# Kernel tuning notes

Measured on AMD Instinct MI355X. Metric: run time of the kernel, lower is better.

## Reference

```python
import jax, jax.numpy as jnp
import numpy as np

B, S, H, NREL = 4, 512, 256, 99


def setup_inputs() -> dict:
    key = jax.random.key(0)
    ks = jax.random.split(key, 6)
    return {
        "queries": jax.random.normal(ks[0], (B, S, H), dtype=jnp.float32),
        "keys": jax.random.normal(ks[1], (B, S, H), dtype=jnp.float32),
        "relations": jax.random.randint(ks[2], (B, S, S), 0, NREL, dtype=jnp.int64),
        "Wq": jax.random.normal(ks[3], (H, H), dtype=jnp.float32) * 0.02,
        "bq": jnp.zeros((H,), dtype=jnp.float32),
        "Wk": jax.random.normal(ks[4], (H, H), dtype=jnp.float32) * 0.02,
        "bk": jnp.zeros((H,), dtype=jnp.float32),
        "rel_emb": jax.random.normal(ks[5], (NREL, H), dtype=jnp.float32) * 0.02,
    }


def reference(queries, keys, relations, Wq, bq, Wk, bk, rel_emb):
    # Linear projections (torch Linear: x @ W.T + b)
    q = queries @ Wq.T + bq        # [B, Sq, H]
    k = keys @ Wk.T + bk           # [B, Sk, H]
    r = rel_emb[relations]         # [B, Sq, Sk, H]

    # single head: qk^T + q . r^T, scaled
    qk = jnp.einsum("bqd,bkd->bqk", q, k)       # [B, Sq, Sk]
    qr = jnp.einsum("bqd,bqkd->bqk", q, r)      # [B, Sq, Sk]
    scale = 1.0 / jnp.sqrt(jnp.asarray(q.shape[-1], q.dtype))
    logits = (qk + qr) * scale
    return jax.nn.softmax(logits, axis=-1)       # squeezed head dim -> [B, Sq, Sk]
```

## Files before the change

kernel.cpp:

```cpp
#include <hip/hip_runtime.h>

typedef __attribute__((ext_vector_type(8))) short bf8;
typedef __attribute__((ext_vector_type(4))) float f4;

#define QBF  0
#define KBF  524288
#define REBF 1048576

static __device__ __forceinline__ short bfr(float x) {
    union { float f; unsigned u; } v; v.f = x;
    return (short)((v.u + 0x7FFF + ((v.u >> 16) & 1)) >> 16);
}
static __device__ __forceinline__ bf8 pack8(float4 a, float4 b) {
    bf8 r;
    r[0] = bfr(a.x); r[1] = bfr(a.y); r[2] = bfr(a.z); r[3] = bfr(a.w);
    r[4] = bfr(b.x); r[5] = bfr(b.y); r[6] = bfr(b.z); r[7] = bfr(b.w);
    return r;
}

__global__ __launch_bounds__(256) void proj_kernel(const float* __restrict__ queries,
                                                   const float* __restrict__ keys,
                                                   const float* __restrict__ bq,
                                                   const float* __restrict__ bk,
                                                   const float* __restrict__ Wq,
                                                   const float* __restrict__ Wk,
                                                   const float* __restrict__ rel_emb,
                                                   short* __restrict__ ws) {
    __shared__ short w_l[64 * 264];
    int blk = blockIdx.x;
    int tid = threadIdx.x;

    if (blk >= 256) {
        int idx = ((blk - 256) * 256 + tid) * 16;
        float4 a = make_float4(0.f, 0.f, 0.f, 0.f), b = a, c = a, d = a;
        if ((idx >> 8) < 99) {
            const float4* s = (const float4*)(rel_emb + idx);
            a = s[0]; b = s[1]; c = s[2]; d = s[3];
        }
        *(bf8*)(ws + REBF + idx) = pack8(a, b);
        *(bf8*)(ws + REBF + idx + 8) = pack8(c, d);
        return;
    }

    int mat = blk >> 7;
    int t = blk & 127;
    int m0 = (t >> 2) * 64;
    int n0 = (t & 3) * 64;
    const float* x = mat ? keys : queries;
    const float* W = mat ? Wk : Wq;
    const float* bias = mat ? bk : bq;
    short* outp = ws + (mat ? KBF : QBF);

    int w = tid >> 6;
    int lane = tid & 63;
    int n15 = lane & 15, quad = lane >> 4;

#pragma unroll
    for (int cc = 0; cc < 8; cc++) {
        int chunk = cc * 256 + tid;
        int row = chunk >> 5, col8 = chunk & 31;
        const float4* s = (const float4*)(W + (n0 + row) * 256 + col8 * 8);
        *(bf8*)&w_l[row * 264 + col8 * 8] = pack8(s[0], s[1]);
    }

    int mrow = m0 + w * 16 + n15;
    bf8 afr[8];
#pragma unroll
    for (int kk = 0; kk < 8; kk++) {
        const float4* ap = (const float4*)(x + mrow * 256 + kk * 32 + quad * 8);
        afr[kk] = pack8(ap[0], ap[1]);
    }
    __syncthreads();

    f4 z = {0.f, 0.f, 0.f, 0.f};
    f4 c[4] = {z, z, z, z};
#pragma unroll
    for (int nt = 0; nt < 4; nt++) {
        const short* wr = &w_l[(nt * 16 + n15) * 264 + quad * 8];
#pragma unroll
        for (int kk = 0; kk < 8; kk++) {
            bf8 bfrag = *(const bf8*)(wr + kk * 32);
            c[nt] = __builtin_amdgcn_mfma_f32_16x16x32_bf16(afr[kk], bfrag, c[nt], 0, 0, 0);
        }
    }

    int mbase = m0 + w * 16 + quad * 4;
#pragma unroll
    for (int nt = 0; nt < 4; nt++) {
        int col = n0 + nt * 16 + n15;
        float bv = bias[col];
#pragma unroll
        for (int reg = 0; reg < 4; reg++)
            outp[(mbase + reg) * 256 + col] = bfr(c[nt][reg] + bv);
    }
}

__global__ __launch_bounds__(512) void attn_kernel(const int* __restrict__ relations,
                                                   const short* __restrict__ ws,
                                                   float* __restrict__ out) {
    __shared__ float qr_l[16][112];
    __shared__ float red_m[16][8];
    __shared__ float red_s[16][8];

    int blk = blockIdx.x;
    int b = blk >> 6;
    int i0 = (blk & 63) * 8;
    int gi0 = b * 512 + i0;
    int w = threadIdx.x >> 6;
    int lane = threadIdx.x & 63;
    int n15 = lane & 15, quad = lane >> 4;
    int j0 = w * 64;

    const int* rb = relations + (gi0 + (quad & 1) * 4) * 512 + j0 + n15;
    int rv[4][4];
#pragma unroll
    for (int reg = 0; reg < 4; reg++)
#pragma unroll
        for (int nt = 0; nt < 4; nt++)
            rv[nt][reg] = rb[reg * 512 + nt * 16];

    const short* qbf = ws + QBF;
    const short* kbf = ws + KBF;
    const short* rebf = ws + REBF;

    int arow = gi0 + (n15 & 7);
    bf8 afr[8];
#pragma unroll
    for (int kk = 0; kk < 8; kk++)
        afr[kk] = *(const bf8*)(qbf + arow * 256 + kk * 32 + quad * 8);

    f4 z = {0.f, 0.f, 0.f, 0.f};
    f4 c[4] = {z, z, z, z};
#pragma unroll
    for (int nt = 0; nt < 4; nt++) {
        int krow = b * 512 + j0 + nt * 16 + n15;
        const short* kr = kbf + krow * 256 + quad * 8;
#pragma unroll
        for (int kk = 0; kk < 8; kk++) {
            bf8 bfrag = *(const bf8*)(kr + kk * 32);
            c[nt] = __builtin_amdgcn_mfma_f32_16x16x32_bf16(afr[kk], bfrag, c[nt], 0, 0, 0);
        }
    }

    if (w < 7) {
        f4 cq = z;
        const short* rr = rebf + (w * 16 + n15) * 256 + quad * 8;
#pragma unroll
        for (int kk = 0; kk < 8; kk++) {
            bf8 bfrag = *(const bf8*)(rr + kk * 32);
            cq = __builtin_amdgcn_mfma_f32_16x16x32_bf16(afr[kk], bfrag, cq, 0, 0, 0);
        }
#pragma unroll
        for (int reg = 0; reg < 4; reg++)
            qr_l[quad * 4 + reg][w * 16 + n15] = cq[reg];
    }
    __syncthreads();

    const float scale = 0.0625f;
    float lg[4][4];
#pragma unroll
    for (int nt = 0; nt < 4; nt++)
#pragma unroll
        for (int reg = 0; reg < 4; reg++)
            lg[nt][reg] = (c[nt][reg] + qr_l[quad * 4 + reg][rv[nt][reg]]) * scale;

    float pm[4];
#pragma unroll
    for (int reg = 0; reg < 4; reg++) {
        float m = fmaxf(fmaxf(lg[0][reg], lg[1][reg]), fmaxf(lg[2][reg], lg[3][reg]));
#pragma unroll
        for (int d = 1; d <= 8; d <<= 1) m = fmaxf(m, __shfl_xor(m, d, 64));
        pm[reg] = m;
    }
    if (n15 == 0)
#pragma unroll
        for (int reg = 0; reg < 4; reg++) red_m[quad * 4 + reg][w] = pm[reg];
    __syncthreads();
    float M[4];
#pragma unroll
    for (int reg = 0; reg < 4; reg++) {
        f4 a0 = *(const f4*)&red_m[quad * 4 + reg][0];
        f4 a1 = *(const f4*)&red_m[quad * 4 + reg][4];
        M[reg] = fmaxf(fmaxf(fmaxf(a0[0], a0[1]), fmaxf(a0[2], a0[3])),
                       fmaxf(fmaxf(a1[0], a1[1]), fmaxf(a1[2], a1[3])));
    }

    float ps[4];
#pragma unroll
    for (int reg = 0; reg < 4; reg++) {
        float s = 0.f;
#pragma unroll
        for (int nt = 0; nt < 4; nt++) {
            float e = __expf(lg[nt][reg] - M[reg]);
            lg[nt][reg] = e;
            s += e;
        }
#pragma unroll
        for (int d = 1; d <= 8; d <<= 1) s += __shfl_xor(s, d, 64);
        ps[reg] = s;
    }
    if (n15 == 0)
#pragma unroll
        for (int reg = 0; reg < 4; reg++) red_s[quad * 4 + reg][w] = ps[reg];
    __syncthreads();
    float inv[4];
#pragma unroll
    for (int reg = 0; reg < 4; reg++) {
        f4 a0 = *(const f4*)&red_s[quad * 4 + reg][0];
        f4 a1 = *(const f4*)&red_s[quad * 4 + reg][4];
        inv[reg] = 1.f / (a0[0] + a0[1] + a0[2] + a0[3] + a1[0] + a1[1] + a1[2] + a1[3]);
    }

    if (quad < 2) {
        float* ob = out + (gi0 + quad * 4) * 512 + j0 + n15;
#pragma unroll
        for (int reg = 0; reg < 4; reg++)
#pragma unroll
            for (int nt = 0; nt < 4; nt++)
                ob[reg * 512 + nt * 16] = lg[nt][reg] * inv[reg];
    }
}

extern "C" void kernel_launch(void* const* d_in, const int* in_sizes, int n_in,
                              void* d_out, int out_size, void* d_ws, size_t ws_size,
                              hipStream_t stream) {
    const float* queries = (const float*)d_in[0];
    const float* keys = (const float*)d_in[1];
    const int* relations = (const int*)d_in[2];
    const float* Wq = (const float*)d_in[3];
    const float* bq = (const float*)d_in[4];
    const float* Wk = (const float*)d_in[5];
    const float* bk = (const float*)d_in[6];
    const float* rel_emb = (const float*)d_in[7];
    short* wss = (short*)d_ws;
    float* out = (float*)d_out;

    hipLaunchKernelGGL(proj_kernel, dim3(263), dim3(256), 0, stream,
                       queries, keys, bq, bk, Wq, Wk, rel_emb, wss);
    hipLaunchKernelGGL(attn_kernel, dim3(256), dim3(512), 0, stream, relations, wss, out);
}
```

Before: 91.98 us.

## Fuse projection and attention kernels into one cooperative launch with grid sync

Merges the projection kernel and the attention/softmax kernel into a single cooperative kernel of 256 blocks x 512 threads. A grid-wide barrier separates the projection phase from the attention phase, and shared memory is reused through a union. The projection work is redistributed so each block of 8 waves covers a 64x64 output tile with 2 n-tiles per wave, and the rel_emb conversion is spread over the first blocks. This removes one kernel launch and its inter-kernel gap, at the cost of a grid sync and the cooperative-launch overhead.

After: 205.2 us. +123.1%, slower.

```diff
diff --git a/kernel.cpp b/kernel.cpp
--- a/kernel.cpp
+++ b/kernel.cpp
@@ -1,4 +1,7 @@
 #include <hip/hip_runtime.h>
+#include <hip/hip_cooperative_groups.h>
+
+namespace cg = cooperative_groups;
 
 typedef __attribute__((ext_vector_type(8))) short bf8;
 typedef __attribute__((ext_vector_type(4))) float f4;
@@ -18,206 +21,211 @@
     return r;
 }
 
-__global__ __launch_bounds__(256) void proj_kernel(const float* __restrict__ queries,
-                                                   const float* __restrict__ keys,
-                                                   const float* __restrict__ bq,
-                                                   const float* __restrict__ bk,
-                                                   const float* __restrict__ Wq,
-                                                   const float* __restrict__ Wk,
-                                                   const float* __restrict__ rel_emb,
-                                                   short* __restrict__ ws) {
-    __shared__ short w_l[64 * 264];
+__global__ __launch_bounds__(512) void fused_kernel(
+    const float* __restrict__ queries, const float* __restrict__ keys,
+    const float* __restrict__ bq, const float* __restrict__ bk,
+    const float* __restrict__ Wq, const float* __restrict__ Wk,
+    const float* __restrict__ rel_emb, const int* __restrict__ relations,
+    short* __restrict__ ws, float* __restrict__ out)
+{
+    __shared__ union SM {
+        short w_l[64 * 264];
+        struct {
+            float qr_l[16][112];
+            float red_m[16][8];
+            float red_s[16][8];
+        } a;
+    } sm;
+
     int blk = blockIdx.x;
     int tid = threadIdx.x;
-
-    if (blk >= 256) {
-        int idx = ((blk - 256) * 256 + tid) * 16;
-        float4 a = make_float4(0.f, 0.f, 0.f, 0.f), b = a, c = a, d = a;
-        if ((idx >> 8) < 99) {
-            const float4* s = (const float4*)(rel_emb + idx);
-            a = s[0]; b = s[1]; c = s[2]; d = s[3];
-        }
-        *(bf8*)(ws + REBF + idx) = pack8(a, b);
-        *(bf8*)(ws + REBF + idx + 8) = pack8(c, d);
-        return;
-    }
-
-    int mat = blk >> 7;
-    int t = blk & 127;
-    int m0 = (t >> 2) * 64;
-    int n0 = (t & 3) * 64;
-    const float* x = mat ? keys : queries;
-    const float* W = mat ? Wk : Wq;
-    const float* bias = mat ? bk : bq;
-    short* outp = ws + (mat ? KBF : QBF);
-
     int w = tid >> 6;
     int lane = tid & 63;
     int n15 = lane & 15, quad = lane >> 4;
 
-#pragma unroll
-    for (int cc = 0; cc < 8; cc++) {
-        int chunk = cc * 256 + tid;
-        int row = chunk >> 5, col8 = chunk & 31;
-        const float4* s = (const float4*)(W + (n0 + row) * 256 + col8 * 8);
-        *(bf8*)&w_l[row * 264 + col8 * 8] = pack8(s[0], s[1]);
+    {
+        int g = blk * 512 + tid;
+        if (g < 1792) {
+            int idx = g * 16;
+            float4 a = make_float4(0.f, 0.f, 0.f, 0.f), b = a, c2 = a, d = a;
+            if ((idx >> 8) < 99) {
+                const float4* s = (const float4*)(rel_emb + idx);
+                a = s[0]; b = s[1]; c2 = s[2]; d = s[3];
+            }
+            *(bf8*)(ws + REBF + idx) = pack8(a, b);
+            *(bf8*)(ws + REBF + idx + 8) = pack8(c2, d);
+        }
     }
 
-    int mrow = m0 + w * 16 + n15;
-    bf8 afr[8];
-#pragma unroll
-    for (int kk = 0; kk < 8; kk++) {
-        const float4* ap = (const float4*)(x + mrow * 256 + kk * 32 + quad * 8);
-        afr[kk] = pack8(ap[0], ap[1]);
+    {
+        int mat = blk >> 7;
+        int t = blk & 127;
+        int m0 = (t >> 2) * 64;
+        int n0 = (t & 3) * 64;
+        const float* x = mat ? keys : queries;
+        const float* W = mat ? Wk : Wq;
+        const float* bias = mat ? bk : bq;
+        short* outp = ws + (mat ? KBF : QBF);
+
+        int wr = w & 3, wc = w >> 2;
+
+#pragma unroll
+        for (int cc = 0; cc < 4; cc++) {
+            int chunk = cc * 512 + tid;
+            int row = chunk >> 5, col8 = chunk & 31;
+            const float4* s = (const float4*)(W + (n0 + row) * 256 + col8 * 8);
+            *(bf8*)&sm.w_l[row * 264 + col8 * 8] = pack8(s[0], s[1]);
+        }
+
+        int mrow = m0 + wr * 16 + n15;
+        bf8 afr[8];
+#pragma unroll
+        for (int kk = 0; kk < 8; kk++) {
+            const float4* ap = (const float4*)(x + mrow * 256 + kk * 32 + quad * 8);
+            afr[kk] = pack8(ap[0], ap[1]);
+        }
+        __syncthreads();
+
+        f4 z = {0.f, 0.f, 0.f, 0.f};
+        f4 c[2] = {z, z};
+#pragma unroll
+        for (int nt = 0; nt < 2; nt++) {
+            const short* wrp = &sm.w_l[(wc * 32 + nt * 16 + n15) * 264 + quad * 8];
+#pragma unroll
+            for (int kk = 0; kk < 8; kk++) {
+                bf8 bfrag = *(const bf8*)(wrp + kk * 32);
+                c[nt] = __builtin_amdgcn_mfma_f32_16x16x32_bf16(afr[kk], bfrag, c[nt], 0, 0, 0);
+            }
+        }
+
+        int mbase = m0 + wr * 16 + quad * 4;
+#pragma unroll
+        for (int nt = 0; nt < 2; nt++) {
+            int col = n0 + wc * 32 + nt * 16 + n15;
+            float bv = bias[col];
+#pragma unroll
+            for (int reg = 0; reg < 4; reg++)
+                outp[(mbase + reg) * 256 + col] = bfr(c[nt][reg] + bv);
+        }
     }
-    __syncthreads();
-
-    f4 z = {0.f, 0.f, 0.f, 0.f};
-    f4 c[4] = {z, z, z, z};
-#pragma unroll
-    for (int nt = 0; nt < 4; nt++) {
-        const short* wr = &w_l[(nt * 16 + n15) * 264 + quad * 8];
-#pragma unroll
-        for (int kk = 0; kk < 8; kk++) {
-            bf8 bfrag = *(const bf8*)(wr + kk * 32);
-            c[nt] = __builtin_amdgcn_mfma_f32_16x16x32_bf16(afr[kk], bfrag, c[nt], 0, 0, 0);
-        }
-    }
-
-    int mbase = m0 + w * 16 + quad * 4;
-#pragma unroll
-    for (int nt = 0; nt < 4; nt++) {
-        int col = n0 + nt * 16 + n15;
-        float bv = bias[col];
+
+    __threadfence();
+    cg::this_grid().sync();
+
+    {
+        int b = blk >> 6;
+        int i0 = (blk & 63) * 8;
+        int gi0 = b * 512 + i0;
+        int j0 = w * 64;
+
+        const int* rb = relations + (gi0 + (quad & 1) * 4) * 512 + j0 + n15;
+        int rv[4][4];
 #pragma unroll
         for (int reg = 0; reg < 4; reg++)
-            outp[(mbase + reg) * 256 + col] = bfr(c[nt][reg] + bv);
-    }
-}
-
-__global__ __launch_bounds__(512) void attn_kernel(const int* __restrict__ relations,
-                                                   const short* __restrict__ ws,
-                                                   float* __restrict__ out) {
-    __shared__ float qr_l[16][112];
-    __shared__ float red_m[16][8];
-    __shared__ float red_s[16][8];
-
-    int blk = blockIdx.x;
-    int b = blk >> 6;
-    int i0 = (blk & 63) * 8;
-    int gi0 = b * 512 + i0;
-    int w = threadIdx.x >> 6;
-    int lane = threadIdx.x & 63;
-    int n15 = lane & 15, quad = lane >> 4;
-    int j0 = w * 64;
-
-    const int* rb = relations + (gi0 + (quad & 1) * 4) * 512 + j0 + n15;
-    int rv[4][4];
-#pragma unroll
-    for (int reg = 0; reg < 4; reg++)
+#pragma unroll
+            for (int nt = 0; nt < 4; nt++)
+                rv[nt][reg] = rb[reg * 512 + nt * 16];
+
+        const short* qbf = ws + QBF;
+        const short* kbf = ws + KBF;
+        const short* rebf = ws + REBF;
+
+        int arow = gi0 + (n15 & 7);
+        bf8 afr[8];
+#pragma unroll
+        for (int kk = 0; kk < 8; kk++)
+            afr[kk] = *(const bf8*)(qbf + arow * 256 + kk * 32 + quad * 8);
+
+        f4 z = {0.f, 0.f, 0.f, 0.f};
+        f4 c[4] = {z, z, z, z};
+#pragma unroll
+        for (int nt = 0; nt < 4; nt++) {
+            int krow = b * 512 + j0 + nt * 16 + n15;
+            const short* kr = kbf + krow * 256 + quad * 8;
+#pragma unroll
+            for (int kk = 0; kk < 8; kk++) {
+                bf8 bfrag = *(const bf8*)(kr + kk * 32);
+                c[nt] = __builtin_amdgcn_mfma_f32_16x16x32_bf16(afr[kk], bfrag, c[nt], 0, 0, 0);
+            }
+        }
+
+        if (w < 7) {
+            f4 cq = z;
+            const short* rr = rebf + (w * 16 + n15) * 256 + quad * 8;
+#pragma unroll
+            for (int kk = 0; kk < 8; kk++) {
+                bf8 bfrag = *(const bf8*)(rr + kk * 32);
+                cq = __builtin_amdgcn_mfma_f32_16x16x32_bf16(afr[kk], bfrag, cq, 0, 0, 0);
+            }
+#pragma unroll
+            for (int reg = 0; reg < 4; reg++)
+                sm.a.qr_l[quad * 4 + reg][w * 16 + n15] = cq[reg];
+        }
+        __syncthreads();
+
+        const float scale = 0.0625f;
+        float lg[4][4];
 #pragma unroll
         for (int nt = 0; nt < 4; nt++)
-            rv[nt][reg] = rb[reg * 512 + nt * 16];
-
-    const short* qbf = ws + QBF;
-    const short* kbf = ws + KBF;
-    const short* rebf = ws + REBF;
-
-    int arow = gi0 + (n15 & 7);
-    bf8 afr[8];
-#pragma unroll
-    for (int kk = 0; kk < 8; kk++)
-        afr[kk] = *(const bf8*)(qbf + arow * 256 + kk * 32 + quad * 8);
-
-    f4 z = {0.f, 0.f, 0.f, 0.f};
-    f4 c[4] = {z, z, z, z};
-#pragma unroll
-    for (int nt = 0; nt < 4; nt++) {
-        int krow = b * 512 + j0 + nt * 16 + n15;
-        const short* kr = kbf + krow * 256 + quad * 8;
-#pragma unroll
-        for (int kk = 0; kk < 8; kk++) {
-            bf8 bfrag = *(const bf8*)(kr + kk * 32);
-            c[nt] = __builtin_amdgcn_mfma_f32_16x16x32_bf16(afr[kk], bfrag, c[nt], 0, 0, 0);
-        }
-    }
-
-    if (w < 7) {
-        f4 cq = z;
-        const short* rr = rebf + (w * 16 + n15) * 256 + quad * 8;
-#pragma unroll
-        for (int kk = 0; kk < 8; kk++) {
-            bf8 bfrag = *(const bf8*)(rr + kk * 32);
-            cq = __builtin_amdgcn_mfma_f32_16x16x32_bf16(afr[kk], bfrag, cq, 0, 0, 0);
-        }
-#pragma unroll
-        for (int reg = 0; reg < 4; reg++)
-            qr_l[quad * 4 + reg][w * 16 + n15] = cq[reg];
-    }
-    __syncthreads();
-
-    const float scale = 0.0625f;
-    float lg[4][4];
-#pragma unroll
-    for (int nt = 0; nt < 4; nt++)
-#pragma unroll
-        for (int reg = 0; reg < 4; reg++)
-            lg[nt][reg] = (c[nt][reg] + qr_l[quad * 4 + reg][rv[nt][reg]]) * scale;
-
-    float pm[4];
-#pragma unroll
-    for (int reg = 0; reg < 4; reg++) {
-        float m = fmaxf(fmaxf(lg[0][reg], lg[1][reg]), fmaxf(lg[2][reg], lg[3][reg]));
-#pragma unroll
-        for (int d = 1; d <= 8; d <<= 1) m = fmaxf(m, __shfl_xor(m, d, 64));
-        pm[reg] = m;
-    }
-    if (n15 == 0)
-#pragma unroll
-        for (int reg = 0; reg < 4; reg++) red_m[quad * 4 + reg][w] = pm[reg];
-    __syncthreads();
-    float M[4];
-#pragma unroll
-    for (int reg = 0; reg < 4; reg++) {
-        f4 a0 = *(const f4*)&red_m[quad * 4 + reg][0];
-        f4 a1 = *(const f4*)&red_m[quad * 4 + reg][4];
-        M[reg] = fmaxf(fmaxf(fmaxf(a0[0], a0[1]), fmaxf(a0[2], a0[3])),
-                       fmaxf(fmaxf(a1[0], a1[1]), fmaxf(a1[2], a1[3])));
-    }
-
-    float ps[4];
-#pragma unroll
-    for (int reg = 0; reg < 4; reg++) {
-        float s = 0.f;
-#pragma unroll
-        for (int nt = 0; nt < 4; nt++) {
-            float e = __expf(lg[nt][reg] - M[reg]);
-            lg[nt][reg] = e;
-            s += e;
-        }
-#pragma unroll
-        for (int d = 1; d <= 8; d <<= 1) s += __shfl_xor(s, d, 64);
-        ps[reg] = s;
-    }
-    if (n15 == 0)
-#pragma unroll
-        for (int reg = 0; reg < 4; reg++) red_s[quad * 4 + reg][w] = ps[reg];
-    __syncthreads();
-    float inv[4];
-#pragma unroll
-    for (int reg = 0; reg < 4; reg++) {
-        f4 a0 = *(const f4*)&red_s[quad * 4 + reg][0];
-        f4 a1 = *(const f4*)&red_s[quad * 4 + reg][4];
-        inv[reg] = 1.f / (a0[0] + a0[1] + a0[2] + a0[3] + a1[0] + a1[1] + a1[2] + a1[3]);
-    }
-
-    if (quad < 2) {
-        float* ob = out + (gi0 + quad * 4) * 512 + j0 + n15;
-#pragma unroll
-        for (int reg = 0; reg < 4; reg++)
-#pragma unroll
-            for (int nt = 0; nt < 4; nt++)
-                ob[reg * 512 + nt * 16] = lg[nt][reg] * inv[reg];
+#pragma unroll
+            for (int reg = 0; reg < 4; reg++)
+                lg[nt][reg] = (c[nt][reg] + sm.a.qr_l[quad * 4 + reg][rv[nt][reg]]) * scale;
+
+        float pm[4];
+#pragma unroll
+        for (int reg = 0; reg < 4; reg++) {
+            float m = fmaxf(fmaxf(lg[0][reg], lg[1][reg]), fmaxf(lg[2][reg], lg[3][reg]));
+#pragma unroll
+            for (int d = 1; d <= 8; d <<= 1) m = fmaxf(m, __shfl_xor(m, d, 64));
+            pm[reg] = m;
+        }
+        if (n15 == 0)
+#pragma unroll
+            for (int reg = 0; reg < 4; reg++) sm.a.red_m[quad * 4 + reg][w] = pm[reg];
+        __syncthreads();
+        float M[4];
+#pragma unroll
+        for (int reg = 0; reg < 4; reg++) {
+            f4 a0 = *(const f4*)&sm.a.red_m[quad * 4 + reg][0];
+            f4 a1 = *(const f4*)&sm.a.red_m[quad * 4 + reg][4];
+            M[reg] = fmaxf(fmaxf(fmaxf(a0[0], a0[1]), fmaxf(a0[2], a0[3])),
+                           fmaxf(fmaxf(a1[0], a1[1]), fmaxf(a1[2], a1[3])));
+        }
+
+        float ps[4];
+#pragma unroll
+        for (int reg = 0; reg < 4; reg++) {
+            float s = 0.f;
+#pragma unroll
+            for (int nt = 0; nt < 4; nt++) {
+                float e = __expf(lg[nt][reg] - M[reg]);
+                lg[nt][reg] = e;
+                s += e;
+            }
+#pragma unroll
+            for (int d = 1; d <= 8; d <<= 1) s += __shfl_xor(s, d, 64);
+            ps[reg] = s;
+        }
+        if (n15 == 0)
+#pragma unroll
+            for (int reg = 0; reg < 4; reg++) sm.a.red_s[quad * 4 + reg][w] = ps[reg];
+        __syncthreads();
+        float inv[4];
+#pragma unroll
+        for (int reg = 0; reg < 4; reg++) {
+            f4 a0 = *(const f4*)&sm.a.red_s[quad * 4 + reg][0];
+            f4 a1 = *(const f4*)&sm.a.red_s[quad * 4 + reg][4];
+            inv[reg] = 1.f / (a0[0] + a0[1] + a0[2] + a0[3] + a1[0] + a1[1] + a1[2] + a1[3]);
+        }
+
+        if (quad < 2) {
+            float* ob = out + (gi0 + quad * 4) * 512 + j0 + n15;
+#pragma unroll
+            for (int reg = 0; reg < 4; reg++)
+#pragma unroll
+                for (int nt = 0; nt < 4; nt++)
+                    ob[reg * 512 + nt * 16] = lg[nt][reg] * inv[reg];
+        }
     }
 }
 
@@ -235,7 +243,8 @@
     short* wss = (short*)d_ws;
     float* out = (float*)d_out;
 
-    hipLaunchKernelGGL(proj_kernel, dim3(263), dim3(256), 0, stream,
-                       queries, keys, bq, bk, Wq, Wk, rel_emb, wss);
-    hipLaunchKernelGGL(attn_kernel, dim3(256), dim3(512), 0, stream, relations, wss, out);
-}
+    void* args[] = {(void*)&queries, (void*)&keys, (void*)&bq, (void*)&bk,
+                    (void*)&Wq, (void*)&Wk, (void*)&rel_emb, (void*)&relations,
+                    (void*)&wss, (void*)&out};
+    hipLaunchCooperativeKernel((void*)fused_kernel, dim3(256), dim3(512), args, 0, stream);
+}
```

## Shrink projection and attention tiles to launch more blocks

Applied to the files above, without the earlier changes.

The projection GEMM moves from 64x64 to 32x32 output tiles, with each of four waves computing one 16x16 tile, so the grid grows from 263 to 1031 blocks. The attention kernel handles 4 query rows per block instead of 8, doubling the grid to 512 blocks. The 4 rows are replicated across the MFMA's 16 rows, and each quad writes the column tile matching its index. The aim is to fill more CUs and cut per-block latency. The cost is redundant MFMA work and about twice the total K/rel-embedding reads from L2.

After: 129.4 us. 40.7% more time.

```diff
diff --git a/kernel.cpp b/kernel.cpp
--- a/kernel.cpp
+++ b/kernel.cpp
@@ -26,12 +26,12 @@
                                                    const float* __restrict__ Wk,
                                                    const float* __restrict__ rel_emb,
                                                    short* __restrict__ ws) {
-    __shared__ short w_l[64 * 264];
+    __shared__ short w_l[32 * 264];
     int blk = blockIdx.x;
     int tid = threadIdx.x;
 
-    if (blk >= 256) {
-        int idx = ((blk - 256) * 256 + tid) * 16;
+    if (blk >= 1024) {
+        int idx = ((blk - 1024) * 256 + tid) * 16;
         float4 a = make_float4(0.f, 0.f, 0.f, 0.f), b = a, c = a, d = a;
         if ((idx >> 8) < 99) {
             const float4* s = (const float4*)(rel_emb + idx);
@@ -42,10 +42,10 @@
         return;
     }
 
-    int mat = blk >> 7;
-    int t = blk & 127;
-    int m0 = (t >> 2) * 64;
-    int n0 = (t & 3) * 64;
+    int mat = blk >> 9;
+    int t = blk & 511;
+    int m0 = (t >> 3) * 32;
+    int n0 = (t & 7) * 32;
     const float* x = mat ? keys : queries;
     const float* W = mat ? Wk : Wq;
     const float* bias = mat ? bk : bq;
@@ -54,16 +54,17 @@
     int w = tid >> 6;
     int lane = tid & 63;
     int n15 = lane & 15, quad = lane >> 4;
-
-#pragma unroll
-    for (int cc = 0; cc < 8; cc++) {
+    int wr = w & 1, wc = w >> 1;
+
+#pragma unroll
+    for (int cc = 0; cc < 4; cc++) {
         int chunk = cc * 256 + tid;
         int row = chunk >> 5, col8 = chunk & 31;
         const float4* s = (const float4*)(W + (n0 + row) * 256 + col8 * 8);
         *(bf8*)&w_l[row * 264 + col8 * 8] = pack8(s[0], s[1]);
     }
 
-    int mrow = m0 + w * 16 + n15;
+    int mrow = m0 + wr * 16 + n15;
     bf8 afr[8];
 #pragma unroll
     for (int kk = 0; kk < 8; kk++) {
@@ -72,27 +73,20 @@
     }
     __syncthreads();
 
-    f4 z = {0.f, 0.f, 0.f, 0.f};
-    f4 c[4] = {z, z, z, z};
-#pragma unroll
-    for (int nt = 0; nt < 4; nt++) {
-        const short* wr = &w_l[(nt * 16 + n15) * 264 + quad * 8];
-#pragma unroll
-        for (int kk = 0; kk < 8; kk++) {
-            bf8 bfrag = *(const bf8*)(wr + kk * 32);
-            c[nt] = __builtin_amdgcn_mfma_f32_16x16x32_bf16(afr[kk], bfrag, c[nt], 0, 0, 0);
-        }
-    }
-
-    int mbase = m0 + w * 16 + quad * 4;
-#pragma unroll
-    for (int nt = 0; nt < 4; nt++) {
-        int col = n0 + nt * 16 + n15;
-        float bv = bias[col];
-#pragma unroll
-        for (int reg = 0; reg < 4; reg++)
-            outp[(mbase + reg) * 256 + col] = bfr(c[nt][reg] + bv);
-    }
+    f4 c = {0.f, 0.f, 0.f, 0.f};
+    const short* wrp = &w_l[(wc * 16 + n15) * 264 + quad * 8];
+#pragma unroll
+    for (int kk = 0; kk < 8; kk++) {
+        bf8 bfrag = *(const bf8*)(wrp + kk * 32);
+        c = __builtin_amdgcn_mfma_f32_16x16x32_bf16(afr[kk], bfrag, c, 0, 0, 0);
+    }
+
+    int mbase = m0 + wr * 16 + quad * 4;
+    int col = n0 + wc * 16 + n15;
+    float bv = bias[col];
+#pragma unroll
+    for (int reg = 0; reg < 4; reg++)
+        outp[(mbase + reg) * 256 + col] = bfr(c[reg] + bv);
 }
 
 __global__ __launch_bounds__(512) void attn_kernel(const int* __restrict__ relations,
@@ -103,15 +97,15 @@
     __shared__ float red_s[16][8];
 
     int blk = blockIdx.x;
-    int b = blk >> 6;
-    int i0 = (blk & 63) * 8;
+    int b = blk >> 7;
+    int i0 = (blk & 127) * 4;
     int gi0 = b * 512 + i0;
     int w = threadIdx.x >> 6;
     int lane = threadIdx.x & 63;
     int n15 = lane & 15, quad = lane >> 4;
     int j0 = w * 64;
 
-    const int* rb = relations + (gi0 + (quad & 1) * 4) * 512 + j0 + n15;
+    const int* rb = relations + gi0 * 512 + j0 + n15;
     int rv[4][4];
 #pragma unroll
     for (int reg = 0; reg < 4; reg++)
@@ -123,7 +117,7 @@
     const short* kbf = ws + KBF;
     const short* rebf = ws + REBF;
 
-    int arow = gi0 + (n15 & 7);
+    int arow = gi0 + (n15 & 3);
     bf8 afr[8];
 #pragma unroll
     for (int kk = 0; kk < 8; kk++)
@@ -211,14 +205,19 @@
         inv[reg] = 1.f / (a0[0] + a0[1] + a0[2] + a0[3] + a1[0] + a1[1] + a1[2] + a1[3]);
     }
 
-    if (quad < 2) {
-        float* ob = out + (gi0 + quad * 4) * 512 + j0 + n15;
-#pragma unroll
-        for (int reg = 0; reg < 4; reg++)
-#pragma unroll
-            for (int nt = 0; nt < 4; nt++)
-                ob[reg * 512 + nt * 16] = lg[nt][reg] * inv[reg];
-    }
+    float sv[4];
+#pragma unroll
+    for (int reg = 0; reg < 4; reg++) {
+        float v = lg[0][reg];
+        if (quad == 1) v = lg[1][reg];
+        if (quad == 2) v = lg[2][reg];
+        if (quad == 3) v = lg[3][reg];
+        sv[reg] = v * inv[reg];
+    }
+    float* ob = out + gi0 * 512 + j0 + quad * 16 + n15;
+#pragma unroll
+    for (int reg = 0; reg < 4; reg++)
+        ob[reg * 512] = sv[reg];
 }
 
 extern "C" void kernel_launch(void* const* d_in, const int* in_sizes, int n_in,
@@ -235,7 +234,7 @@
     short* wss = (short*)d_ws;
     float* out = (float*)d_out;
 
-    hipLaunchKernelGGL(proj_kernel, dim3(263), dim3(256), 0, stream,
+    hipLaunchKernelGGL(proj_kernel, dim3(1031), dim3(256), 0, stream,
                        queries, keys, bq, bk, Wq, Wk, rel_emb, wss);
-    hipLaunchKernelGGL(attn_kernel, dim3(256), dim3(512), 0, stream, relations, wss, out);
-}
+    hipLaunchKernelGGL(attn_kernel, dim3(512), dim3(512), 0, stream, relations, wss, out);
+}
```
